# Optimization experiments

Hardware: AMD Instinct MI355X
Metric: run time of the kernel (lower is better)

## Reference

```python
import jax, jax.numpy as jnp
import numpy as np

# ---- dims (match init_kwargs) ----
B0, C0, H0, W0 = 16, 64, 128, 128
G = 8            # d_model of inner Mamba2
D_STATE = 16
D_CONV = 3
EXPAND = 2
HEADDIM = 8
D_INNER = EXPAND * G            # 16
NHEADS = D_INNER // HEADDIM     # 2
NGROUPS = 1
CONV_DIM = D_INNER + 2 * NGROUPS * D_STATE   # 48
D_IN_PROJ = 2 * D_INNER + 2 * NGROUPS * D_STATE + NHEADS  # 66
EPS = 1e-5


def silu(x):
    return x * jax.nn.sigmoid(x)


def setup_inputs() -> dict:
    key = jax.random.key(0)
    ks = jax.random.split(key, 12)
    s = 0.02
    return {
        "x": jax.random.normal(ks[0], (B0, C0, H0, W0), jnp.float32),
        # 1x1 conv tokenize / detokenize (stored as matrices)
        "w_tok": jax.random.normal(ks[1], (G, C0), jnp.float32) * s,
        "b_tok": jnp.zeros((G,), jnp.float32),
        "w_detok": jax.random.normal(ks[2], (C0, G), jnp.float32) * s,
        "b_detok": jnp.zeros((C0,), jnp.float32),
        # Mamba2 params
        "w_in": jax.random.normal(ks[3], (D_IN_PROJ, G), jnp.float32) * s,
        "w_conv": jax.random.normal(ks[4], (CONV_DIM, 1, D_CONV), jnp.float32) * s,
        "b_conv": jnp.zeros((CONV_DIM,), jnp.float32),
        "dt_bias": jax.random.uniform(ks[5], (NHEADS,), jnp.float32, -4.0, -2.0),
        "A_log": jnp.log(jnp.arange(1, NHEADS + 1, dtype=jnp.float32)),
        "D": jnp.ones((NHEADS,), jnp.float32),
        "norm_w": jnp.ones((D_INNER,), jnp.float32),
        "w_out": jax.random.normal(ks[6], (G, D_INNER), jnp.float32) * s,
    }


def _mamba2(u, w_in, w_conv, b_conv, dt_bias, A_log, D, norm_w, w_out):
    # u: [B, L, G]
    Bb, L, _ = u.shape
    zxbcdt = jnp.einsum('blg,dg->bld', u, w_in)                 # [B,L,66]
    z = zxbcdt[..., :D_INNER]                                   # [B,L,16]
    xBC = zxbcdt[..., D_INNER:D_INNER + CONV_DIM]               # [B,L,48]
    dt = jax.nn.softplus(zxbcdt[..., D_INNER + CONV_DIM:] + dt_bias)  # [B,L,H]

    # causal depthwise conv1d over time
    xBC_t = jnp.moveaxis(xBC, 1, 2)                             # [B,48,L]
    xBC_t = jnp.pad(xBC_t, ((0, 0), (0, 0), (D_CONV - 1, 0)))
    xBC_t = jax.lax.conv_general_dilated(
        xBC_t, w_conv, window_strides=(1,), padding='VALID',
        dimension_numbers=('NCH', 'OIH', 'NCH'), feature_group_count=CONV_DIM)
    xBC = silu(jnp.moveaxis(xBC_t + b_conv[None, :, None], 1, 2))  # [B,L,48]

    xh = xBC[..., :D_INNER].reshape(Bb, L, NHEADS, HEADDIM)     # [B,L,H,P]
    Bm = xBC[..., D_INNER:D_INNER + D_STATE]                    # [B,L,N] (ngroups=1)
    Cm = xBC[..., D_INNER + D_STATE:]                           # [B,L,N]

    A = -jnp.exp(A_log)                                         # [H]
    dA = jnp.exp(dt * A)                                        # [B,L,H]

    # time-major sequential selective scan
    def step(state, inp):
        dA_t, dt_t, x_t, B_t, C_t = inp  # [B,H],[B,H],[B,H,P],[B,N],[B,N]
        state = state * dA_t[:, :, None, None] \
            + (dt_t[:, :, None] * x_t)[..., None] * B_t[:, None, None, :]
        y = jnp.einsum('bhpn,bn->bhp', state, C_t)
        return state, y

    init = jnp.zeros((Bb, NHEADS, HEADDIM, D_STATE), u.dtype)
    xs = (jnp.moveaxis(dA, 1, 0), jnp.moveaxis(dt, 1, 0),
          jnp.moveaxis(xh, 1, 0), jnp.moveaxis(Bm, 1, 0), jnp.moveaxis(Cm, 1, 0))
    _, ys = jax.lax.scan(step, init, xs)                        # [L,B,H,P]
    y = jnp.moveaxis(ys, 0, 1) + D[None, None, :, None] * xh    # [B,L,H,P]
    y = y.reshape(Bb, L, D_INNER)

    # gated RMSNorm then out projection
    y = y * silu(z)
    y = y * jax.lax.rsqrt(jnp.mean(y * y, axis=-1, keepdims=True) + EPS) * norm_w
    return jnp.einsum('bld,gd->blg', y, w_out)


def reference(x, w_tok, b_tok, w_detok, b_detok, w_in, w_conv, b_conv,
              dt_bias, A_log, D, norm_w, w_out):
    Bb, C, H, W = x.shape
    g = jnp.einsum('bchw,gc->bghw', x, w_tok) + b_tok[None, :, None, None]
    g = g.reshape(Bb, G, H * W).transpose(0, 2, 1)              # [B,HW,G]
    g = _mamba2(g, w_in, w_conv, b_conv, dt_bias, A_log, D, norm_w, w_out) + g
    g = g.transpose(0, 2, 1).reshape(Bb, G, H, W)
    return x + jnp.einsum('bghw,cg->bchw', g, w_detok) + b_detok[None, :, None, None]
```

## Files before the change

### kernel.cpp

```cpp
#include <hip/hip_runtime.h>

namespace {
constexpr int NB   = 16;
constexpr int NC   = 64;
constexpr int HW   = 128*128;
constexpr int SL   = 16384;
constexpr int CQ   = 64;
constexpr int NCH  = SL/CQ;
constexpr int PWV  = 11776;

typedef short short8 __attribute__((ext_vector_type(8)));
typedef float f32x4  __attribute__((ext_vector_type(4)));

__device__ __forceinline__ float frcp(float x){ return __builtin_amdgcn_rcpf(x); }
__device__ __forceinline__ float rl(float v, int s){
  return __int_as_float(__builtin_amdgcn_readlane(__float_as_int(v), s));
}
__device__ __forceinline__ float sigu(float a){ return frcp(1.0f + __expf(-a)); }
__device__ __forceinline__ float softplusf(float a){
  return fmaxf(a, 0.f) + __logf(1.f + __expf(-fabsf(a)));
}
__device__ __forceinline__ unsigned bfr(float x){
  unsigned u = __float_as_uint(x);
  u = u + 0x7FFF + ((u>>16)&1);
  return u>>16;
}
__device__ __forceinline__ unsigned pk2(float a, float b){
  return (bfr(a)&0xFFFFu) | (bfr(b)<<16);
}
__device__ __forceinline__ float blo(unsigned u){ return __uint_as_float(u<<16); }
__device__ __forceinline__ float bhi(unsigned u){ return __uint_as_float(u & 0xFFFF0000u); }
union CV8 { unsigned u[4]; short8 s; };

__global__ __launch_bounds__(256) void k_tok(
    const float* __restrict__ x, const float* __restrict__ w_tok,
    const float* __restrict__ b_tok, float* __restrict__ g0)
{
  __shared__ float s_wt[NC][8];
  __shared__ float s_bt[8];
  for (int i = threadIdx.x; i < NC*8; i += 256) s_wt[i>>3][i&7] = w_tok[(i&7)*NC + (i>>3)];
  if (threadIdx.x < 8) s_bt[threadIdx.x] = b_tok[threadIdx.x];
  __syncthreads();
  long idx = (long)blockIdx.x * 256 + threadIdx.x;
  int b = (int)(idx >> 14);
  int l = (int)(idx & (SL-1));
  float acc[8];
  #pragma unroll
  for (int g = 0; g < 8; ++g) acc[g] = s_bt[g];
  const float* xp = x + (long)b*NC*HW + l;
  #pragma unroll 8
  for (int c = 0; c < NC; ++c) {
    float v = xp[(long)c*HW];
    const float4* wr = (const float4*)s_wt[c];
    float4 w0 = wr[0], w1 = wr[1];
    acc[0] += v*w0.x; acc[1] += v*w0.y; acc[2] += v*w0.z; acc[3] += v*w0.w;
    acc[4] += v*w1.x; acc[5] += v*w1.y; acc[6] += v*w1.z; acc[7] += v*w1.w;
  }
  float* gp = g0 + idx*8;
  *(float4*)gp     = make_float4(acc[0],acc[1],acc[2],acc[3]);
  *(float4*)(gp+4) = make_float4(acc[4],acc[5],acc[6],acc[7]);
}

__global__ __launch_bounds__(256) void k_front(
    const float* __restrict__ g0, const float* __restrict__ w_in,
    const float* __restrict__ w_conv, const float* __restrict__ b_conv,
    const float* __restrict__ dt_bias, const float* __restrict__ A_log,
    const float* __restrict__ Dvec,
    float* __restrict__ Sc, float* __restrict__ Pc,
    float* __restrict__ ceg, unsigned short* __restrict__ Cg,
    float* __restrict__ Yg)
{
  __shared__ short s_weff[64*32];
  __shared__ float s_bc[48];
  __shared__ float s_misc[8];
  __shared__ char  s_wv[4][PWV];

  int tid = threadIdx.x, lane = tid & 63, wave = tid >> 6;
  int c15 = lane & 15, lg = lane >> 4;

  for (int i = tid; i < 64*32; i += 256) {
    int j = i >> 5, k = i & 31;
    float v = 0.f;
    if (j < 48) {
      if (k < 24) v = w_conv[j*3 + (k>>3)] * w_in[(16+j)*8 + (k&7)];
    } else if (j < 50) {
      if (k >= 16 && k < 24) v = w_in[(64 + (j-48))*8 + (k-16)];
    }
    s_weff[i] = (short)bfr(v);
  }
  if (tid < 48) s_bc[tid] = b_conv[tid];
  if (tid < 2) {
    s_misc[tid]   = -__expf(A_log[tid]);
    s_misc[2+tid] = dt_bias[tid];
    s_misc[4+tid] = Dvec[tid];
  }
  __syncthreads();

  int b   = blockIdx.x >> 6;
  int chB = (blockIdx.x & 63)*4 + wave;
  long cg = (long)b*NCH + chB;
  int l0  = chB*CQ;
  char* WR = s_wv[wave];
  char* BT  = WR;
  char* uB  = WR + 2048;
  char* uC  = WR + 4096;
  char* Mb  = WR;
  char* ytr = WR;
  char* Xp  = WR + 8192;
  char* dtL = WR + 10240;
  char* cfL = WR + 10752;
  char* ceL = WR + 11264;

  short8 zero8 = {0,0,0,0,0,0,0,0};
  f32x4  zero4 = {0.f,0.f,0.f,0.f};

  short8 Af[4];
  #pragma unroll
  for (int tt = 0; tt < 4; ++tt) {
    int p = l0 + 16*tt + c15 - 2 + lg;
    bool ok = (lg < 3) && (p >= 0);
    const float* up = g0 + ((long)b*SL + (ok ? p : 0))*8;
    float4 a = *(const float4*)up, c = *(const float4*)(up+4);
    CV8 w;
    w.u[0] = pk2(a.x,a.y); w.u[1] = pk2(a.z,a.w);
    w.u[2] = pk2(c.x,c.y); w.u[3] = pk2(c.z,c.w);
    Af[tt] = ok ? w.s : zero8;
  }

  f32x4 xg[4];
  #pragma unroll
  for (int jj = 0; jj < 4; ++jj) {
    short8 Wf = *(const short8*)(s_weff + (16*jj + c15)*32 + lg*8);
    f32x4 o[4];
    #pragma unroll
    for (int tt = 0; tt < 4; ++tt)
      o[tt] = __builtin_amdgcn_mfma_f32_16x16x32_bf16(Af[tt], Wf, zero4, 0,0,0);
    if (jj == 3) {
      if (c15 < 2) {
        float bias = s_misc[2+c15];
        #pragma unroll
        for (int tt = 0; tt < 4; ++tt) {
          #pragma unroll
          for (int r = 0; r < 4; ++r)
            *(float*)(dtL + c15*256 + (16*tt + 4*lg + r)*4) = o[tt][r] + bias;
        }
      }
    } else {
      float bias = s_bc[16*jj + c15];
      #pragma unroll
      for (int tt = 0; tt < 4; ++tt) {
        float s0 = (o[tt][0]+bias), s1 = (o[tt][1]+bias);
        float s2 = (o[tt][2]+bias), s3 = (o[tt][3]+bias);
        s0 *= sigu(s0); s1 *= sigu(s1); s2 *= sigu(s2); s3 *= sigu(s3);
        int t0 = 16*tt + 4*lg;
        if (jj == 0) {
          f32x4 v; v[0]=s0; v[1]=s1; v[2]=s2; v[3]=s3;
          xg[tt] = v;
        } else if (jj == 1) {
          uint2 wv; wv.x = pk2(s0,s1); wv.y = pk2(s2,s3);
          *(uint2*)(BT + c15*128 + ((t0*2) ^ ((c15&7)<<4))) = wv;
          *(short*)(uB + (t0  )*32 + c15*2) = (short)bfr(s0);
          *(short*)(uB + (t0+1)*32 + c15*2) = (short)bfr(s1);
          *(short*)(uB + (t0+2)*32 + c15*2) = (short)bfr(s2);
          *(short*)(uB + (t0+3)*32 + c15*2) = (short)bfr(s3);
        } else {
          *(short*)(uC + (t0  )*32 + c15*2) = (short)bfr(s0);
          *(short*)(uC + (t0+1)*32 + c15*2) = (short)bfr(s1);
          *(short*)(uC + (t0+2)*32 + c15*2) = (short)bfr(s2);
          *(short*)(uC + (t0+3)*32 + c15*2) = (short)bfr(s3);
        }
      }
    }
  }
  __builtin_amdgcn_wave_barrier();
  __builtin_amdgcn_sched_barrier(0x7F);

  float dt0 = softplusf(*(const float*)(dtL + lane*4));
  float dt1 = softplusf(*(const float*)(dtL + 256 + lane*4));
  float c0 = s_misc[0]*dt0, c1 = s_misc[1]*dt1;
  #pragma unroll
  for (int off = 1; off < 64; off <<= 1) {
    float t0 = __shfl_up(c0, off), t1 = __shfl_up(c1, off);
    if (lane >= off) { c0 += t0; c1 += t1; }
  }
  float ce0 = __expf(c0), ce1 = __expf(c1);
  float cf0 = __expf(-c0)*dt0, cf1 = __expf(-c1)*dt1;
  float cee0 = rl(ce0, 63), cee1 = rl(ce1, 63);
  ceg[cg*128 + lane]      = ce0;
  ceg[cg*128 + 64 + lane] = ce1;
  if (lane == 0) { Pc[cg*2] = cee0; Pc[cg*2+1] = cee1; }
  *(float*)(cfL + lane*4)       = cf0;
  *(float*)(cfL + 256 + lane*4) = cf1;
  *(float*)(ceL + lane*4)       = ce0;
  *(float*)(ceL + 256 + lane*4) = ce1;
  __builtin_amdgcn_wave_barrier();
  __builtin_amdgcn_sched_barrier(0x7F);

  int hh = (c15 < 8) ? 0 : 1;
  #pragma unroll
  for (int tt = 0; tt < 4; ++tt) {
    int t0 = 16*tt + 4*lg;
    float4 cf4 = *(const float4*)(cfL + hh*256 + t0*4);
    uint2 wv;
    wv.x = pk2(cf4.x*xg[tt][0], cf4.y*xg[tt][1]);
    wv.y = pk2(cf4.z*xg[tt][2], cf4.w*xg[tt][3]);
    *(uint2*)(Xp + c15*128 + ((t0*2) ^ ((c15&7)<<4))) = wv;
  }
  __builtin_amdgcn_wave_barrier();
  __builtin_amdgcn_sched_barrier(0x7F);

  { short8 ca = *(const short8*)(uC + lane*32);
    short8 cb = *(const short8*)(uC + lane*32 + 16);
    *(short8*)(Cg + cg*1024 + lane*16)     = ca;
    *(short8*)(Cg + cg*1024 + lane*16 + 8) = cb; }

  { f32x4 sacc = zero4;
    #pragma unroll
    for (int kb = 0; kb < 2; ++kb) {
      int cb2 = (64*kb + 16*lg) ^ ((c15&7)<<4);
      short8 Afx = *(const short8*)(Xp + c15*128 + cb2);
      short8 Bfx = *(const short8*)(BT + c15*128 + cb2);
      sacc = __builtin_amdgcn_mfma_f32_16x16x32_bf16(Afx, Bfx, sacc, 0,0,0);
    }
    float cee = (lg < 2) ? cee0 : cee1;
    #pragma unroll
    for (int r = 0; r < 4; ++r)
      Sc[cg*256 + (4*lg+r)*16 + c15] = cee*sacc[r];
  }

  short8 Cfr[4], Bfr[4], Xf[2];
  #pragma unroll
  for (int tt = 0; tt < 4; ++tt) {
    Cfr[tt] = zero8; Bfr[tt] = zero8;
    if (lg < 2) {
      Cfr[tt] = *(const short8*)(uC + (16*tt + c15)*32 + 16*lg);
      Bfr[tt] = *(const short8*)(uB + (16*tt + c15)*32 + 16*lg);
    }
  }
  #pragma unroll
  for (int kb = 0; kb < 2; ++kb)
    Xf[kb] = *(const short8*)(Xp + c15*128 + ((64*kb + 16*lg) ^ ((c15&7)<<4)));
  __builtin_amdgcn_wave_barrier();
  __builtin_amdgcn_sched_barrier(0x7F);

  #pragma unroll
  for (int tt = 0; tt < 4; ++tt) {
    int t  = 16*tt + c15;
    int sw = (t&7)<<4;
    #pragma unroll
    for (int ts = 0; ts < 4; ++ts) {
      if (ts <= tt) {
        f32x4 gA = __builtin_amdgcn_mfma_f32_16x16x32_bf16(Bfr[ts], Cfr[tt], zero4, 0,0,0);
        if (ts == tt) {
          #pragma unroll
          for (int r = 0; r < 4; ++r)
            gA[r] = (4*lg + r <= c15) ? gA[r] : 0.f;
        }
        uint2 wv; wv.x = pk2(gA[0],gA[1]); wv.y = pk2(gA[2],gA[3]);
        *(uint2*)(Mb + t*128 + ((32*ts + 8*lg) ^ sw)) = wv;
      }
    }
    if (tt == 0 || tt == 2) {
      uint2 zv; zv.x = 0u; zv.y = 0u;
      *(uint2*)(Mb + t*128 + ((32*(tt+1) + 8*lg) ^ sw)) = zv;
    }
  }
  __builtin_amdgcn_wave_barrier();
  __builtin_amdgcn_sched_barrier(0x7F);

  f32x4 acc[4];
  #pragma unroll
  for (int tt = 0; tt < 4; ++tt) acc[tt] = zero4;
  #pragma unroll
  for (int tt = 0; tt < 4; ++tt) {
    int t = 16*tt + c15, sw = (t&7)<<4;
    { short8 Mf = *(const short8*)(Mb + t*128 + ((16*lg) ^ sw));
      acc[tt] = __builtin_amdgcn_mfma_f32_16x16x32_bf16(Mf, Xf[0], acc[tt], 0,0,0); }
    if (tt >= 2) {
      short8 Mf = *(const short8*)(Mb + t*128 + ((64 + 16*lg) ^ sw));
      acc[tt] = __builtin_amdgcn_mfma_f32_16x16x32_bf16(Mf, Xf[1], acc[tt], 0,0,0);
    }
  }
  __builtin_amdgcn_sched_barrier(0x7F);

  float Dh = (c15 < 8) ? s_misc[4] : s_misc[5];
  #pragma unroll
  for (int tt = 0; tt < 4; ++tt) {
    int t0 = 16*tt + 4*lg;
    float4 ce4 = *(const float4*)(ceL + hh*256 + t0*4);
    *(float*)(ytr + (t0  )*96 + c15*4) = ce4.x*acc[tt][0] + Dh*xg[tt][0];
    *(float*)(ytr + (t0+1)*96 + c15*4) = ce4.y*acc[tt][1] + Dh*xg[tt][1];
    *(float*)(ytr + (t0+2)*96 + c15*4) = ce4.z*acc[tt][2] + Dh*xg[tt][2];
    *(float*)(ytr + (t0+3)*96 + c15*4) = ce4.w*acc[tt][3] + Dh*xg[tt][3];
  }
  __builtin_amdgcn_wave_barrier();
  __builtin_amdgcn_sched_barrier(0x7F);

  float* yg = Yg + cg*1024 + lane*16;
  #pragma unroll
  for (int i = 0; i < 4; ++i) {
    float4 q = *(const float4*)(ytr + lane*96 + i*16);
    *(float4*)(yg + 4*i) = q;
  }
}

__global__ __launch_bounds__(256) void k_scan(
    const float* __restrict__ Sc, const float* __restrict__ Pc,
    float* __restrict__ Stin)
{
  int b = blockIdx.x;
  int tid = threadIdx.x;
  int h = tid >> 7;
  float st = 0.f;
  long base = (long)b * NCH;
  #pragma unroll 8
  for (int c = 0; c < NCH; ++c) {
    Stin[(base + c)*256 + tid] = st;
    st = st * Pc[(base + c)*2 + h] + Sc[(base + c)*256 + tid];
  }
}

__global__ __launch_bounds__(256) void k_apply(
    const float* __restrict__ g0, const float* __restrict__ w_in,
    const float* __restrict__ norm_w, const float* __restrict__ w_out,
    const float* __restrict__ Stin, const float* __restrict__ ceg,
    const unsigned short* __restrict__ Cg, const float* __restrict__ Yg,
    float* __restrict__ gf)
{
  __shared__ float s_win[16][8];
  __shared__ float s_wout[8][16];
  __shared__ float s_nw[16];
  __shared__ float s_st[4][256];

  int tid = threadIdx.x, lane = tid & 63, wave = tid >> 6;
  if (tid < 128) s_win[tid>>3][tid&7] = w_in[tid];
  if (tid < 128) s_wout[tid>>4][tid&15] = w_out[tid];
  if (tid < 16)  s_nw[tid] = norm_w[tid];
  __syncthreads();

  auto dot8 = [&](const float* uu, int row) -> float {
    const float4* wr = (const float4*)s_win[row];
    float4 w0 = wr[0], w1 = wr[1];
    return uu[0]*w0.x + uu[1]*w0.y + uu[2]*w0.z + uu[3]*w0.w
         + uu[4]*w1.x + uu[5]*w1.y + uu[6]*w1.z + uu[7]*w1.w;
  };

  int b   = blockIdx.x >> 6;
  int chB = (blockIdx.x & 63)*4 + wave;
  long cg = (long)b*NCH + chB;
  long pos = (long)b*SL + chB*CQ + lane;

  { float4 t4 = *(const float4*)(Stin + cg*256 + lane*4);
    *(float4*)&s_st[wave][lane*4] = t4; }

  float u[8];
  { const float* up = g0 + pos*8;
    float4 a = *(const float4*)up, c = *(const float4*)(up+4);
    u[0]=a.x;u[1]=a.y;u[2]=a.z;u[3]=a.w;u[4]=c.x;u[5]=c.y;u[6]=c.z;u[7]=c.w; }

  float Cr[16];
  { const uint4* cp = (const uint4*)(Cg + cg*1024 + lane*16);
    uint4 ca = cp[0], cb = cp[1];
    Cr[0]=blo(ca.x); Cr[1]=bhi(ca.x); Cr[2]=blo(ca.y); Cr[3]=bhi(ca.y);
    Cr[4]=blo(ca.z); Cr[5]=bhi(ca.z); Cr[6]=blo(ca.w); Cr[7]=bhi(ca.w);
    Cr[8]=blo(cb.x); Cr[9]=bhi(cb.x); Cr[10]=blo(cb.y); Cr[11]=bhi(cb.y);
    Cr[12]=blo(cb.z); Cr[13]=bhi(cb.z); Cr[14]=blo(cb.w); Cr[15]=bhi(cb.w); }

  float yr[16];
  { const float* yp = Yg + cg*1024 + lane*16;
    #pragma unroll
    for (int i = 0; i < 4; ++i) {
      float4 q = *(const float4*)(yp + 4*i);
      yr[4*i]=q.x; yr[4*i+1]=q.y; yr[4*i+2]=q.z; yr[4*i+3]=q.w;
    } }
  float ce0t = ceg[cg*128 + lane];
  float ce1t = ceg[cg*128 + 64 + lane];

  __builtin_amdgcn_wave_barrier();
  __builtin_amdgcn_sched_barrier(0x7F);

  const float* st = &s_st[wave][0];
  float y[16];
  #pragma unroll
  for (int hp = 0; hp < 16; ++hp) {
    const float4* sp = (const float4*)(st + hp*16);
    float4 s0 = sp[0], s1 = sp[1], s2 = sp[2], s3 = sp[3];
    float a = Cr[0]*s0.x + Cr[1]*s0.y + Cr[2]*s0.z + Cr[3]*s0.w
            + Cr[4]*s1.x + Cr[5]*s1.y + Cr[6]*s1.z + Cr[7]*s1.w
            + Cr[8]*s2.x + Cr[9]*s2.y + Cr[10]*s2.z + Cr[11]*s2.w
            + Cr[12]*s3.x + Cr[13]*s3.y + Cr[14]*s3.z + Cr[15]*s3.w;
    y[hp] = yr[hp] + ((hp < 8) ? ce0t : ce1t)*a;
  }

  float yv[16]; float ss = 0.f;
  #pragma unroll
  for (int d = 0; d < 16; ++d) {
    float zz = dot8(u, d);
    float v = y[d] * (zz * sigu(zz));
    yv[d] = v; ss += v*v;
  }
  float scn = rsqrtf(ss*(1.f/16.f) + 1e-5f);
  { const float4* nw = (const float4*)s_nw;
    float4 n0 = nw[0], n1 = nw[1], n2 = nw[2], n3 = nw[3];
    yv[0]*=scn*n0.x; yv[1]*=scn*n0.y; yv[2]*=scn*n0.z; yv[3]*=scn*n0.w;
    yv[4]*=scn*n1.x; yv[5]*=scn*n1.y; yv[6]*=scn*n1.z; yv[7]*=scn*n1.w;
    yv[8]*=scn*n2.x; yv[9]*=scn*n2.y; yv[10]*=scn*n2.z; yv[11]*=scn*n2.w;
    yv[12]*=scn*n3.x; yv[13]*=scn*n3.y; yv[14]*=scn*n3.z; yv[15]*=scn*n3.w; }
  float og[8];
  #pragma unroll
  for (int g = 0; g < 8; ++g) {
    const float4* wr = (const float4*)s_wout[g];
    float4 w0 = wr[0], w1 = wr[1], w2 = wr[2], w3 = wr[3];
    float a = u[g];
    a += yv[0]*w0.x + yv[1]*w0.y + yv[2]*w0.z + yv[3]*w0.w;
    a += yv[4]*w1.x + yv[5]*w1.y + yv[6]*w1.z + yv[7]*w1.w;
    a += yv[8]*w2.x + yv[9]*w2.y + yv[10]*w2.z + yv[11]*w2.w;
    a += yv[12]*w3.x + yv[13]*w3.y + yv[14]*w3.z + yv[15]*w3.w;
    og[g] = a;
  }
  float* gp = gf + pos*8;
  *(float4*)gp     = make_float4(og[0],og[1],og[2],og[3]);
  *(float4*)(gp+4) = make_float4(og[4],og[5],og[6],og[7]);
}

__global__ __launch_bounds__(256) void k_detok(
    const float* __restrict__ x, const float* __restrict__ gf,
    const float* __restrict__ w_detok, const float* __restrict__ b_detok,
    float* __restrict__ out)
{
  __shared__ float s_wd[NC][8];
  __shared__ float s_bd[NC];
  for (int i = threadIdx.x; i < NC*8; i += 256) s_wd[i>>3][i&7] = w_detok[i];
  if (threadIdx.x < NC) s_bd[threadIdx.x] = b_detok[threadIdx.x];
  __syncthreads();
  long idx = (long)blockIdx.x * 256 + threadIdx.x;
  int b = (int)(idx >> 14);
  int l = (int)(idx & (SL-1));
  float gv[8];
  const float* gp = gf + idx*8;
  { float4 a = *(const float4*)gp, c = *(const float4*)(gp+4);
    gv[0]=a.x;gv[1]=a.y;gv[2]=a.z;gv[3]=a.w;gv[4]=c.x;gv[5]=c.y;gv[6]=c.z;gv[7]=c.w; }
  const float* xp = x + (long)b*NC*HW + l;
  float* op = out + (long)b*NC*HW + l;
  #pragma unroll 4
  for (int c = 0; c < NC; ++c) {
    const float4* wr = (const float4*)s_wd[c];
    float4 w0 = wr[0], w1 = wr[1];
    float a = s_bd[c] + xp[(long)c*HW];
    a += gv[0]*w0.x + gv[1]*w0.y + gv[2]*w0.z + gv[3]*w0.w;
    a += gv[4]*w1.x + gv[5]*w1.y + gv[6]*w1.z + gv[7]*w1.w;
    op[(long)c*HW] = a;
  }
}
}

extern "C" void kernel_launch(void* const* d_in, const int* in_sizes, int n_in,
                              void* d_out, int out_size, void* d_ws, size_t ws_size,
                              hipStream_t stream)
{
  const float* x       = (const float*)d_in[0];
  const float* w_tok   = (const float*)d_in[1];
  const float* b_tok   = (const float*)d_in[2];
  const float* w_detok = (const float*)d_in[3];
  const float* b_detok = (const float*)d_in[4];
  const float* w_in    = (const float*)d_in[5];
  const float* w_conv  = (const float*)d_in[6];
  const float* b_conv  = (const float*)d_in[7];
  const float* dt_bias = (const float*)d_in[8];
  const float* A_log   = (const float*)d_in[9];
  const float* Dvec    = (const float*)d_in[10];
  const float* norm_w  = (const float*)d_in[11];
  const float* w_out   = (const float*)d_in[12];
  float* out = (float*)d_out;

  float* ws   = (float*)d_ws;
  float* g0   = ws;
  float* gf   = g0 + (long)NB*SL*8;
  float* Sc   = gf + (long)NB*SL*8;
  float* Pc   = Sc + (long)NB*NCH*256;
  float* Stin = Pc + (long)NB*NCH*2;
  float* ceg  = Stin + (long)NB*NCH*256;
  float* Yg   = ceg + (long)NB*NCH*128;
  unsigned short* Cg = (unsigned short*)(Yg + (long)NB*NCH*1024);

  k_tok<<<NB*SL/256, 256, 0, stream>>>(x, w_tok, b_tok, g0);
  k_front<<<NB*NCH/4, 256, 0, stream>>>(g0, w_in, w_conv, b_conv, dt_bias,
                                        A_log, Dvec, Sc, Pc, ceg, Cg, Yg);
  k_scan<<<NB, 256, 0, stream>>>(Sc, Pc, Stin);
  k_apply<<<NB*NCH/4, 256, 0, stream>>>(g0, w_in, norm_w, w_out,
                                        Stin, ceg, Cg, Yg, gf);
  k_detok<<<NB*SL/256, 256, 0, stream>>>(x, gf, w_detok, b_detok, out);
}
```

Baseline: 101.9 us.

## Fuse detokenize into apply kernel and precompute conv-projection weights once

Merges the detokenization pass into the apply kernel, so the intermediate gf buffer (16x16384x8 floats) is no longer written and read back, and one kernel launch is removed. Separately, the fused conv/in-projection bf16 weight matrix is now built once by block 0 of the tokenize kernel and stored in global memory, instead of being rebuilt into LDS by every k_front block. This shrinks k_front's LDS use, which may allow more blocks per CU, but it reads the weights from global memory inside the MFMA loop. The fused output kernel now handles 64 channel writes per position, which makes it heavier and may reduce its parallelism.

```diff
diff --git a/kernel.cpp b/kernel.cpp
--- a/kernel.cpp
+++ b/kernel.cpp
@@ -7,7 +7,7 @@
 constexpr int SL   = 16384;
 constexpr int CQ   = 64;
 constexpr int NCH  = SL/CQ;
-constexpr int PWV  = 11776;
+constexpr int PWV  = 9728;
 
 typedef short short8 __attribute__((ext_vector_type(8)));
 typedef float f32x4  __attribute__((ext_vector_type(4)));
@@ -34,8 +34,22 @@
 
 __global__ __launch_bounds__(256) void k_tok(
     const float* __restrict__ x, const float* __restrict__ w_tok,
-    const float* __restrict__ b_tok, float* __restrict__ g0)
+    const float* __restrict__ b_tok, float* __restrict__ g0,
+    const float* __restrict__ w_in, const float* __restrict__ w_conv,
+    unsigned short* __restrict__ weff)
 {
+  if (blockIdx.x == 0) {
+    for (int i = threadIdx.x; i < 64*32; i += 256) {
+      int j = i >> 5, k = i & 31;
+      float v = 0.f;
+      if (j < 48) {
+        if (k < 24) v = w_conv[j*3 + (k>>3)] * w_in[(16+j)*8 + (k&7)];
+      } else if (j < 50) {
+        if (k >= 16 && k < 24) v = w_in[(64 + (j-48))*8 + (k-16)];
+      }
+      weff[i] = (unsigned short)bfr(v);
+    }
+  }
   __shared__ float s_wt[NC][8];
   __shared__ float s_bt[8];
   for (int i = threadIdx.x; i < NC*8; i += 256) s_wt[i>>3][i&7] = w_tok[(i&7)*NC + (i>>3)];
@@ -62,15 +76,14 @@
 }
 
 __global__ __launch_bounds__(256) void k_front(
-    const float* __restrict__ g0, const float* __restrict__ w_in,
-    const float* __restrict__ w_conv, const float* __restrict__ b_conv,
+    const float* __restrict__ g0, const unsigned short* __restrict__ weff,
+    const float* __restrict__ b_conv,
     const float* __restrict__ dt_bias, const float* __restrict__ A_log,
     const float* __restrict__ Dvec,
     float* __restrict__ Sc, float* __restrict__ Pc,
     float* __restrict__ ceg, unsigned short* __restrict__ Cg,
     float* __restrict__ Yg)
 {
-  __shared__ short s_weff[64*32];
   __shared__ float s_bc[48];
   __shared__ float s_misc[8];
   __shared__ char  s_wv[4][PWV];
@@ -78,16 +91,6 @@
   int tid = threadIdx.x, lane = tid & 63, wave = tid >> 6;
   int c15 = lane & 15, lg = lane >> 4;
 
-  for (int i = tid; i < 64*32; i += 256) {
-    int j = i >> 5, k = i & 31;
-    float v = 0.f;
-    if (j < 48) {
-      if (k < 24) v = w_conv[j*3 + (k>>3)] * w_in[(16+j)*8 + (k&7)];
-    } else if (j < 50) {
-      if (k >= 16 && k < 24) v = w_in[(64 + (j-48))*8 + (k-16)];
-    }
-    s_weff[i] = (short)bfr(v);
-  }
   if (tid < 48) s_bc[tid] = b_conv[tid];
   if (tid < 2) {
     s_misc[tid]   = -__expf(A_log[tid]);
@@ -104,12 +107,12 @@
   char* BT  = WR;
   char* uB  = WR + 2048;
   char* uC  = WR + 4096;
+  char* Xp  = WR + 6144;
   char* Mb  = WR;
   char* ytr = WR;
-  char* Xp  = WR + 8192;
-  char* dtL = WR + 10240;
-  char* cfL = WR + 10752;
-  char* ceL = WR + 11264;
+  char* dtL = WR + 8192;
+  char* cfL = WR + 8704;
+  char* ceL = WR + 9216;
 
   short8 zero8 = {0,0,0,0,0,0,0,0};
   f32x4  zero4 = {0.f,0.f,0.f,0.f};
@@ -130,7 +133,7 @@
   f32x4 xg[4];
   #pragma unroll
   for (int jj = 0; jj < 4; ++jj) {
-    short8 Wf = *(const short8*)(s_weff + (16*jj + c15)*32 + lg*8);
+    short8 Wf = *(const short8*)(weff + (16*jj + c15)*32 + lg*8);
     f32x4 o[4];
     #pragma unroll
     for (int tt = 0; tt < 4; ++tt)
@@ -320,22 +323,27 @@
   }
 }
 
-__global__ __launch_bounds__(256) void k_apply(
+__global__ __launch_bounds__(256) void k_out(
     const float* __restrict__ g0, const float* __restrict__ w_in,
     const float* __restrict__ norm_w, const float* __restrict__ w_out,
     const float* __restrict__ Stin, const float* __restrict__ ceg,
     const unsigned short* __restrict__ Cg, const float* __restrict__ Yg,
-    float* __restrict__ gf)
+    const float* __restrict__ x, const float* __restrict__ w_detok,
+    const float* __restrict__ b_detok, float* __restrict__ out)
 {
   __shared__ float s_win[16][8];
   __shared__ float s_wout[8][16];
   __shared__ float s_nw[16];
+  __shared__ float s_wd[NC][8];
+  __shared__ float s_bd[NC];
   __shared__ float s_st[4][256];
 
   int tid = threadIdx.x, lane = tid & 63, wave = tid >> 6;
   if (tid < 128) s_win[tid>>3][tid&7] = w_in[tid];
   if (tid < 128) s_wout[tid>>4][tid&15] = w_out[tid];
   if (tid < 16)  s_nw[tid] = norm_w[tid];
+  for (int i = tid; i < NC*8; i += 256) s_wd[i>>3][i&7] = w_detok[i];
+  if (tid < NC) s_bd[tid] = b_detok[tid];
   __syncthreads();
 
   auto dot8 = [&](const float* uu, int row) -> float {
@@ -348,7 +356,8 @@
   int b   = blockIdx.x >> 6;
   int chB = (blockIdx.x & 63)*4 + wave;
   long cg = (long)b*NCH + chB;
-  long pos = (long)b*SL + chB*CQ + lane;
+  int l   = chB*CQ + lane;
+  long pos = (long)b*SL + l;
 
   { float4 t4 = *(const float4*)(Stin + cg*256 + lane*4);
     *(float4*)&s_st[wave][lane*4] = t4; }
@@ -418,28 +427,7 @@
     a += yv[12]*w3.x + yv[13]*w3.y + yv[14]*w3.z + yv[15]*w3.w;
     og[g] = a;
   }
-  float* gp = gf + pos*8;
-  *(float4*)gp     = make_float4(og[0],og[1],og[2],og[3]);
-  *(float4*)(gp+4) = make_float4(og[4],og[5],og[6],og[7]);
-}
-
-__global__ __launch_bounds__(256) void k_detok(
-    const float* __restrict__ x, const float* __restrict__ gf,
-    const float* __restrict__ w_detok, const float* __restrict__ b_detok,
-    float* __restrict__ out)
-{
-  __shared__ float s_wd[NC][8];
-  __shared__ float s_bd[NC];
-  for (int i = threadIdx.x; i < NC*8; i += 256) s_wd[i>>3][i&7] = w_detok[i];
-  if (threadIdx.x < NC) s_bd[threadIdx.x] = b_detok[threadIdx.x];
-  __syncthreads();
-  long idx = (long)blockIdx.x * 256 + threadIdx.x;
-  int b = (int)(idx >> 14);
-  int l = (int)(idx & (SL-1));
-  float gv[8];
-  const float* gp = gf + idx*8;
-  { float4 a = *(const float4*)gp, c = *(const float4*)(gp+4);
-    gv[0]=a.x;gv[1]=a.y;gv[2]=a.z;gv[3]=a.w;gv[4]=c.x;gv[5]=c.y;gv[6]=c.z;gv[7]=c.w; }
+
   const float* xp = x + (long)b*NC*HW + l;
   float* op = out + (long)b*NC*HW + l;
   #pragma unroll 4
@@ -447,8 +435,8 @@
     const float4* wr = (const float4*)s_wd[c];
     float4 w0 = wr[0], w1 = wr[1];
     float a = s_bd[c] + xp[(long)c*HW];
-    a += gv[0]*w0.x + gv[1]*w0.y + gv[2]*w0.z + gv[3]*w0.w;
-    a += gv[4]*w1.x + gv[5]*w1.y + gv[6]*w1.z + gv[7]*w1.w;
+    a += og[0]*w0.x + og[1]*w0.y + og[2]*w0.z + og[3]*w0.w;
+    a += og[4]*w1.x + og[5]*w1.y + og[6]*w1.z + og[7]*w1.w;
     op[(long)c*HW] = a;
   }
 }
@@ -475,19 +463,19 @@
 
   float* ws   = (float*)d_ws;
   float* g0   = ws;
-  float* gf   = g0 + (long)NB*SL*8;
-  float* Sc   = gf + (long)NB*SL*8;
+  float* Sc   = g0 + (long)NB*SL*8;
   float* Pc   = Sc + (long)NB*NCH*256;
   float* Stin = Pc + (long)NB*NCH*2;
   float* ceg  = Stin + (long)NB*NCH*256;
   float* Yg   = ceg + (long)NB*NCH*128;
   unsigned short* Cg = (unsigned short*)(Yg + (long)NB*NCH*1024);
-
-  k_tok<<<NB*SL/256, 256, 0, stream>>>(x, w_tok, b_tok, g0);
-  k_front<<<NB*NCH/4, 256, 0, stream>>>(g0, w_in, w_conv, b_conv, dt_bias,
+  unsigned short* weff = Cg + (long)NB*NCH*1024;
+
+  k_tok<<<NB*SL/256, 256, 0, stream>>>(x, w_tok, b_tok, g0, w_in, w_conv, weff);
+  k_front<<<NB*NCH/4, 256, 0, stream>>>(g0, weff, b_conv, dt_bias,
                                         A_log, Dvec, Sc, Pc, ceg, Cg, Yg);
   k_scan<<<NB, 256, 0, stream>>>(Sc, Pc, Stin);
-  k_apply<<<NB*NCH/4, 256, 0, stream>>>(g0, w_in, norm_w, w_out,
-                                        Stin, ceg, Cg, Yg, gf);
-  k_detok<<<NB*SL/256, 256, 0, stream>>>(x, gf, w_detok, b_detok, out);
-}
+  k_out<<<NB*NCH/4, 256, 0, stream>>>(g0, w_in, norm_w, w_out,
+                                      Stin, ceg, Cg, Yg,
+                                      x, w_detok, b_detok, out);
+}
```

Result: faster. 94.18 us (-7.6%).
